# Optimization experiments

Hardware: AMD Instinct MI355X
Metric: run time of the kernel (lower is better)

Reference implementation:

```python
import jax, jax.numpy as jnp
import numpy as np

B, S, HID, NH, HD = 2, 2048, 768, 12, 64
WINDOW = 128           # ModernBERT local attention window
ROPE_THETA = 10000.0   # local_rope_theta (layer_index=0 -> is_local_attention=True)


def _rotate_half(x):
    x1, x2 = jnp.split(x, 2, axis=-1)
    return jnp.concatenate([-x2, x1], axis=-1)


def setup_inputs() -> dict:
    key = jax.random.key(0)
    k1, k2, k3 = jax.random.split(key, 3)
    hidden_embed = jax.random.normal(k1, (B, S, HID), dtype=jnp.float32)
    Wq = jax.random.normal(k2, (HID, HID), dtype=jnp.float32) * (HID ** -0.5)
    Wo = jax.random.normal(k3, (HID, HID), dtype=jnp.float32) * (HID ** -0.5)
    position_index = jnp.arange(S, dtype=jnp.int32).reshape(1, S)
    # sliding-window additive mask: 0 inside window, -inf outside
    i = jnp.arange(S)
    dist = jnp.abs(i[:, None] - i[None, :])
    local_attention_mask = jnp.where(dist <= WINDOW // 2, 0.0, -jnp.inf).astype(jnp.float32)[None, None]
    global_attention_mask = jnp.zeros((1, 1, S, S), dtype=jnp.float32)
    return {
        "hidden_embed": hidden_embed,
        "Wq": Wq,
        "Wo": Wo,
        "local_attention_mask": local_attention_mask,
        "global_attention_mask": global_attention_mask,
        "position_index": position_index,
    }


def reference(hidden_embed, Wq, Wo, local_attention_mask, global_attention_mask, position_index):
    # q projection; NOTE: source has k = q.view(...), v = q.view(...) -> k and v ARE q
    q = hidden_embed @ Wq.T                                  # [B,S,HID]
    q = q.reshape(B, S, NH, HD).transpose(0, 2, 1, 3)        # [B,NH,S,HD]

    # RoPE
    inv_freq = 1.0 / (ROPE_THETA ** (jnp.arange(0, HD, 2, dtype=jnp.float32) / HD))  # [HD/2]
    pos = position_index.reshape(-1).astype(jnp.float32)     # [S]
    freqs = pos[:, None] * inv_freq[None, :]                 # [S,HD/2]
    emb = jnp.concatenate([freqs, freqs], axis=-1)           # [S,HD]
    cos, sin = jnp.cos(emb), jnp.sin(emb)
    q_rot = q * cos + _rotate_half(q) * sin                  # [B,NH,S,HD]
    k_rot = q_rot                                            # k == q before rope -> same after rope
    v = q                                                    # v == q (no rope on v)

    # masked SDPA (local layer -> local sliding-window mask)
    scale = jnp.asarray(HD, jnp.float32) ** -0.5
    scores = jnp.einsum('bhtd,bhsd->bhts', q_rot, k_rot) * scale + local_attention_mask
    attn = jax.nn.softmax(scores, axis=-1)                   # [B,NH,S,S]
    out = jnp.einsum('bhts,bhsd->bhtd', attn, v)             # [B,NH,S,HD]
    out = out.transpose(0, 2, 1, 3).reshape(B, S, HID)
    return out @ Wo.T
```

## Files before the change

### kernel.cpp

```cpp
#include <hip/hip_runtime.h>
#include <hip/hip_bf16.h>
#include <math.h>
#include <stdint.h>

#define B_    2
#define S_    2048
#define HID_  768
#define NH_   12
#define HD_   64
#define NROWS (B_ * S_)
#define N_HID_ELEM (NROWS * HID_)
#define N_W_ELEM   (HID_ * HID_)

#define KW   224
#define KSTR 232

#define TAB_ELEMS (S_ * 32)

typedef __bf16 bf16x8 __attribute__((ext_vector_type(8)));
typedef float  floatx4 __attribute__((ext_vector_type(4)));

__global__ void convert_inputs_kernel(const float* __restrict__ src_hidden,
                                      const float* __restrict__ src_w1,
                                      const float* __restrict__ src_w2,
                                      const int*   __restrict__ pos_idx,
                                      __hip_bfloat16* __restrict__ Hb,
                                      __hip_bfloat16* __restrict__ Wqb,
                                      __hip_bfloat16* __restrict__ Wob,
                                      float2* __restrict__ tab)
{
    int i = blockIdx.x * blockDim.x + threadIdx.x;
    const int NH4 = N_HID_ELEM / 4, NW4 = N_W_ELEM / 4;
    const int total4 = NH4 + 2 * NW4;
    if (i < total4) {
        const float* src;
        __hip_bfloat16* dst;
        int off;
        if (i < NH4)           { src = src_hidden; dst = Hb;  off = i; }
        else if (i < NH4+NW4)  { src = src_w1;     dst = Wqb; off = i - NH4; }
        else                   { src = src_w2;     dst = Wob; off = i - NH4 - NW4; }
        float4 v = reinterpret_cast<const float4*>(src)[off];
        __hip_bfloat16 o[4] = { __float2bfloat16(v.x), __float2bfloat16(v.y),
                                __float2bfloat16(v.z), __float2bfloat16(v.w) };
        *reinterpret_cast<uint64_t*>(dst + 4 * (size_t)off) = *reinterpret_cast<uint64_t*>(o);
    } else {
        int t = i - total4;
        if (t < TAB_ELEMS) {
            int s = t >> 5, f = t & 31;
            float inv = exp2f((float)f * (-0.41524101186092024f));
            float sn, cs;
            sincosf((float)pos_idx[s] * inv, &sn, &cs);
            tab[t] = make_float2(cs, sn);
        }
    }
}

__device__ __forceinline__ void gload_lds16(const __hip_bfloat16* g, __hip_bfloat16* l)
{
    __builtin_amdgcn_global_load_lds(
        (const __attribute__((address_space(1))) void*)g,
        (__attribute__((address_space(3))) void*)l, 16, 0, 0);
}

template<int ROPE>
__global__ __launch_bounds__(512) void gemm64k2(
    const __hip_bfloat16* __restrict__ A,
    const __hip_bfloat16* __restrict__ W,
    __hip_bfloat16* __restrict__ C,
    __hip_bfloat16* __restrict__ C2,
    float* __restrict__ Cf,
    const float2* __restrict__ tab,
    int M, int N, int K)
{
    __shared__ __align__(16) __hip_bfloat16 Ald[2][2][2][64][32];
    __shared__ __align__(16) __hip_bfloat16 Wld[2][2][2][64][32];

    const int tid  = threadIdx.x;
    const int kg   = tid >> 8;
    const int wv4  = (tid >> 6) & 3;
    const int lane = tid & 63;
    const int l16  = lane & 15;
    const int quad = lane >> 4;
    const int m0 = blockIdx.x * 64;
    const int n0 = blockIdx.y * 64;

    const int c    = wv4 * 64 + lane;
    const int sr   = c >> 2;
    const int sc8  = ((c & 3) ^ ((sr >> 1) & 3)) * 8;
    const int kbase = kg * 384;

    const __hip_bfloat16* gA = A + (size_t)(m0 + sr) * K + kbase + sc8;
    const __hip_bfloat16* gW = W + (size_t)(n0 + sr) * K + kbase + sc8;

    floatx4 acc[4] = {};
    const int ra  = wv4 * 16 + l16;
    const int qsw = (quad ^ ((l16 >> 1) & 3)) * 8;

#define STAGE(itx, buf) do {                                          \
        const int ko_ = (itx) * 64;                                   \
        gload_lds16(gA + ko_,      &Ald[kg][buf][0][wv4 * 16][0]);    \
        gload_lds16(gA + ko_ + 32, &Ald[kg][buf][1][wv4 * 16][0]);    \
        gload_lds16(gW + ko_,      &Wld[kg][buf][0][wv4 * 16][0]);    \
        gload_lds16(gW + ko_ + 32, &Wld[kg][buf][1][wv4 * 16][0]);    \
    } while (0)

    STAGE(0, 0);
    STAGE(1, 1);

#pragma unroll
    for (int it = 0; it < 6; ++it) {
        const int cur = it & 1;
        if (it == 5) { asm volatile("s_waitcnt vmcnt(0)" ::: "memory"); }
        else         { asm volatile("s_waitcnt vmcnt(4)" ::: "memory"); }
        __builtin_amdgcn_s_barrier();
        __builtin_amdgcn_sched_barrier(0);
#pragma unroll
        for (int ks = 0; ks < 2; ++ks) {
            bf16x8 a = *reinterpret_cast<const bf16x8*>(&Ald[kg][cur][ks][ra][qsw]);
#pragma unroll
            for (int u = 0; u < 4; ++u) {
                bf16x8 w = *reinterpret_cast<const bf16x8*>(
                    &Wld[kg][cur][ks][u * 16 + l16][qsw]);
                acc[u] = __builtin_amdgcn_mfma_f32_16x16x32_bf16(a, w, acc[u], 0, 0, 0);
            }
        }
        __builtin_amdgcn_sched_barrier(0);
        __builtin_amdgcn_s_barrier();
        if (it + 2 < 6) STAGE(it + 2, cur);
    }
#undef STAGE

    __syncthreads();
    float* Red = reinterpret_cast<float*>(&Ald[0][0][0][0][0]);
    if (kg == 1) {
#pragma unroll
        for (int u = 0; u < 4; ++u)
#pragma unroll
            for (int r = 0; r < 4; ++r)
                Red[(wv4 * 16 + quad * 4 + r) * 68 + u * 16 + l16] = acc[u][r];
    }
    __syncthreads();
    if (kg == 1) return;
#pragma unroll
    for (int u = 0; u < 4; ++u)
#pragma unroll
        for (int r = 0; r < 4; ++r)
            acc[u][r] += Red[(wv4 * 16 + quad * 4 + r) * 68 + u * 16 + l16];

    if (ROPE) {
#pragma unroll
        for (int r = 0; r < 4; ++r) {
            int m = m0 + wv4 * 16 + quad * 4 + r;
            int s = m & (S_ - 1);
#pragma unroll
            for (int u = 0; u < 2; ++u) {
                float2 cssn = tab[s * 32 + u * 16 + l16];
                float cs = cssn.x, sn = cssn.y;
                float q0 = acc[u][r];
                float q1 = acc[u + 2][r];
                size_t base = (size_t)m * HID_ + n0 + u * 16 + l16;
                C [base]      = __float2bfloat16(q0);
                C [base + 32] = __float2bfloat16(q1);
                C2[base]      = __float2bfloat16(q0 * cs - q1 * sn);
                C2[base + 32] = __float2bfloat16(q1 * cs + q0 * sn);
            }
        }
    } else {
#pragma unroll
        for (int u = 0; u < 4; ++u)
#pragma unroll
            for (int r = 0; r < 4; ++r) {
                int row = m0 + wv4 * 16 + quad * 4 + r;
                int col = n0 + u * 16 + l16;
                Cf[(size_t)row * N + col] = acc[u][r];
            }
    }
}

__global__ __launch_bounds__(256) void attn_kernel(
    const __hip_bfloat16* __restrict__ Q,
    const __hip_bfloat16* __restrict__ Qr,
    __hip_bfloat16* __restrict__ O)
{
    __shared__ __align__(16) __hip_bfloat16 Vt[64][KSTR];
    __shared__ __align__(16) __hip_bfloat16 Pl[64][KSTR];

    const int bh = blockIdx.y;
    const int b  = bh / NH_;
    const int h  = bh % NH_;
    const int i0 = blockIdx.x * 64;
    const int tid = threadIdx.x;

    if (tid < KW) {
        int j  = i0 - 64 + tid;
        int jc = min(max(j, 0), S_ - 1);
        const __hip_bfloat16* vrow = Q + ((size_t)(b * S_ + jc)) * HID_ + h * HD_;
#pragma unroll
        for (int d8i = 0; d8i < 8; ++d8i) {
            bf16x8 v = *reinterpret_cast<const bf16x8*>(vrow + d8i * 8);
            const __hip_bfloat16* ve = reinterpret_cast<const __hip_bfloat16*>(&v);
#pragma unroll
            for (int e = 0; e < 8; ++e) Vt[d8i * 8 + e][tid] = ve[e];
        }
    }
    __syncthreads();

    const int wv   = tid >> 6;
    const int lane = tid & 63;
    const int l16  = lane & 15;
    const int quad = lane >> 4;

    floatx4 sc[10] = {};
    const __hip_bfloat16* qrow =
        Qr + ((size_t)(b * S_ + i0 + wv * 16 + l16)) * HID_ + h * HD_ + quad * 8;
#pragma unroll
    for (int ks = 0; ks < 2; ++ks) {
        bf16x8 a = *reinterpret_cast<const bf16x8*>(qrow + ks * 32);
#pragma unroll
        for (int t = 0; t < 10; ++t) {
            int j = i0 - 64 + (wv + t) * 16 + l16;
            int jc = min(max(j, 0), S_ - 1);
            bf16x8 bfr = *reinterpret_cast<const bf16x8*>(
                Qr + ((size_t)(b * S_ + jc)) * HID_ + h * HD_ + ks * 32 + quad * 8);
            sc[t] = __builtin_amdgcn_mfma_f32_16x16x32_bf16(a, bfr, sc[t], 0, 0, 0);
        }
    }

    const float scale = 0.125f;
    float denom[4];
#pragma unroll
    for (int r = 0; r < 4; ++r) {
        const int R = wv * 16 + quad * 4 + r;
        float xv[10];
        float mx = -3.0e38f;
#pragma unroll
        for (int t = 0; t < 10; ++t) {
            int w = (wv + t) * 16 + l16;
            int j = i0 - 64 + w;
            bool valid = (w >= R) && (w <= R + 128) && (j >= 0) && (j < S_);
            float x = valid ? sc[t][r] * scale : -1.0e30f;
            xv[t] = x;
            mx = fmaxf(mx, x);
        }
#pragma unroll
        for (int msk = 1; msk < 16; msk <<= 1) mx = fmaxf(mx, __shfl_xor(mx, msk, 64));
        float sum = 0.f;
#pragma unroll
        for (int t = 0; t < 10; ++t) {
            float p = __expf(xv[t] - mx);
            sum += p;
            Pl[R][(wv + t) * 16 + l16] = __float2bfloat16(p);
        }
#pragma unroll
        for (int msk = 1; msk < 16; msk <<= 1) sum += __shfl_xor(sum, msk, 64);
        denom[r] = sum;
    }
    __syncthreads();

    floatx4 oacc[4] = {};
#pragma unroll
    for (int c = 0; c < 5; ++c) {
        const int base = wv * 16 + c * 32;
        bf16x8 a = *reinterpret_cast<const bf16x8*>(&Pl[wv * 16 + l16][base + quad * 8]);
#pragma unroll
        for (int u = 0; u < 4; ++u) {
            bf16x8 bfr = *reinterpret_cast<const bf16x8*>(&Vt[u * 16 + l16][base + quad * 8]);
            oacc[u] = __builtin_amdgcn_mfma_f32_16x16x32_bf16(a, bfr, oacc[u], 0, 0, 0);
        }
    }

    __syncthreads();
    float* Of = reinterpret_cast<float*>(&Pl[0][0]);
#pragma unroll
    for (int u = 0; u < 4; ++u)
#pragma unroll
        for (int r = 0; r < 4; ++r)
            Of[(wv * 16 + quad * 4 + r) * 68 + u * 16 + l16] = oacc[u][r] / denom[r];
    __syncthreads();
    {
        int row = tid >> 2;
        int seg = (tid & 3) * 16;
        __hip_bfloat16 ob[16];
#pragma unroll
        for (int e = 0; e < 16; ++e)
            ob[e] = __float2bfloat16(Of[row * 68 + seg + e]);
        __hip_bfloat16* dst = O + ((size_t)(b * S_ + i0 + row)) * HID_ + h * HD_ + seg;
        *reinterpret_cast<bf16x8*>(dst)     = *reinterpret_cast<bf16x8*>(ob);
        *reinterpret_cast<bf16x8*>(dst + 8) = *reinterpret_cast<bf16x8*>(ob + 8);
    }
}

extern "C" void kernel_launch(void* const* d_in, const int* in_sizes, int n_in,
                              void* d_out, int out_size, void* d_ws, size_t ws_size,
                              hipStream_t stream)
{
    int ih = -1, iw1 = -1, iw2 = -1, ip = -1;
    for (int i = 0; i < n_in; ++i) {
        int s = in_sizes[i];
        if      (s == N_HID_ELEM && ih < 0) ih = i;
        else if (s == N_W_ELEM)  { if (iw1 < 0) iw1 = i; else if (iw2 < 0) iw2 = i; }
        else if (s == S_ && ip < 0) ip = i;
    }
    if (ih < 0)  ih = 0;
    if (iw1 < 0) iw1 = 1;
    if (iw2 < 0) iw2 = 2;
    if (ip < 0)  ip = 5;

    const float* hidden = (const float*)d_in[ih];
    const float* w1     = (const float*)d_in[iw1];
    const float* w2     = (const float*)d_in[iw2];
    const int*   pos    = (const int*)d_in[ip];

    __hip_bfloat16* Hb  = (__hip_bfloat16*)d_ws;
    __hip_bfloat16* Wqb = Hb  + N_HID_ELEM;
    __hip_bfloat16* Wob = Wqb + N_W_ELEM;
    __hip_bfloat16* Q   = Wob + N_W_ELEM;
    __hip_bfloat16* Qr  = Q   + N_HID_ELEM;
    float2*         Tab = reinterpret_cast<float2*>(Qr + N_HID_ELEM);
    __hip_bfloat16* AO  = Hb;

    int conv4 = (N_HID_ELEM + 2 * N_W_ELEM) / 4;
    int convtot = conv4 + TAB_ELEMS;
    convert_inputs_kernel<<<(convtot + 255) / 256, 256, 0, stream>>>(
        hidden, w1, w2, pos, Hb, Wqb, Wob, Tab);

    dim3 gblk(NROWS / 64, HID_ / 64);

    gemm64k2<1><<<gblk, 512, 0, stream>>>(Hb, Wqb, Q, Qr, nullptr, Tab,
                                          NROWS, HID_, HID_);

    attn_kernel<<<dim3(S_ / 64, B_ * NH_), 256, 0, stream>>>(Q, Qr, AO);

    gemm64k2<0><<<gblk, 512, 0, stream>>>(AO, Wob, nullptr, nullptr, (float*)d_out,
                                          nullptr, NROWS, HID_, HID_);
}
```

Baseline: 139.6 us.

## Fuse fp32-to-bf16 conversion and RoPE table into GEMM kernels

Removes the separate conversion kernel: both GEMMs now load fp32 weights (and fp32 hidden for the Q projection) directly from global memory into registers, convert them to bf16, and write to LDS, with register prefetch replacing async global-to-LDS loads. The RoPE cos/sin table is computed per block in shared memory, and block indices are remapped to group tiles for L2 reuse. This saves one launch and a full bf16 round-trip through memory, at the cost of fetching twice the bytes per GEMM tile, redundant weight conversion across blocks, and extra sincos work per block.

```diff
diff --git a/kernel.cpp b/kernel.cpp
--- a/kernel.cpp
+++ b/kernel.cpp
@@ -15,65 +15,32 @@
 #define KW   224
 #define KSTR 232
 
-#define TAB_ELEMS (S_ * 32)
-
 typedef __bf16 bf16x8 __attribute__((ext_vector_type(8)));
 typedef float  floatx4 __attribute__((ext_vector_type(4)));
 
-__global__ void convert_inputs_kernel(const float* __restrict__ src_hidden,
-                                      const float* __restrict__ src_w1,
-                                      const float* __restrict__ src_w2,
-                                      const int*   __restrict__ pos_idx,
-                                      __hip_bfloat16* __restrict__ Hb,
-                                      __hip_bfloat16* __restrict__ Wqb,
-                                      __hip_bfloat16* __restrict__ Wob,
-                                      float2* __restrict__ tab)
+__device__ __forceinline__ void cvt_write8(const float4& x, const float4& y,
+                                           __hip_bfloat16* d)
 {
-    int i = blockIdx.x * blockDim.x + threadIdx.x;
-    const int NH4 = N_HID_ELEM / 4, NW4 = N_W_ELEM / 4;
-    const int total4 = NH4 + 2 * NW4;
-    if (i < total4) {
-        const float* src;
-        __hip_bfloat16* dst;
-        int off;
-        if (i < NH4)           { src = src_hidden; dst = Hb;  off = i; }
-        else if (i < NH4+NW4)  { src = src_w1;     dst = Wqb; off = i - NH4; }
-        else                   { src = src_w2;     dst = Wob; off = i - NH4 - NW4; }
-        float4 v = reinterpret_cast<const float4*>(src)[off];
-        __hip_bfloat16 o[4] = { __float2bfloat16(v.x), __float2bfloat16(v.y),
-                                __float2bfloat16(v.z), __float2bfloat16(v.w) };
-        *reinterpret_cast<uint64_t*>(dst + 4 * (size_t)off) = *reinterpret_cast<uint64_t*>(o);
-    } else {
-        int t = i - total4;
-        if (t < TAB_ELEMS) {
-            int s = t >> 5, f = t & 31;
-            float inv = exp2f((float)f * (-0.41524101186092024f));
-            float sn, cs;
-            sincosf((float)pos_idx[s] * inv, &sn, &cs);
-            tab[t] = make_float2(cs, sn);
-        }
-    }
+    __hip_bfloat16 t[8] = { __float2bfloat16(x.x), __float2bfloat16(x.y),
+                            __float2bfloat16(x.z), __float2bfloat16(x.w),
+                            __float2bfloat16(y.x), __float2bfloat16(y.y),
+                            __float2bfloat16(y.z), __float2bfloat16(y.w) };
+    *reinterpret_cast<bf16x8*>(d) = *reinterpret_cast<bf16x8*>(t);
 }
 
-__device__ __forceinline__ void gload_lds16(const __hip_bfloat16* g, __hip_bfloat16* l)
-{
-    __builtin_amdgcn_global_load_lds(
-        (const __attribute__((address_space(1))) void*)g,
-        (__attribute__((address_space(3))) void*)l, 16, 0, 0);
-}
-
-template<int ROPE>
-__global__ __launch_bounds__(512) void gemm64k2(
-    const __hip_bfloat16* __restrict__ A,
-    const __hip_bfloat16* __restrict__ W,
+template<int ROPE, int AF32>
+__global__ __launch_bounds__(512, 4) void gemm64f(
+    const void*  __restrict__ Asrc,
+    const float* __restrict__ Wf,
     __hip_bfloat16* __restrict__ C,
     __hip_bfloat16* __restrict__ C2,
     float* __restrict__ Cf,
-    const float2* __restrict__ tab,
-    int M, int N, int K)
+    const int* __restrict__ pos_idx)
 {
+    constexpr int K = HID_;
     __shared__ __align__(16) __hip_bfloat16 Ald[2][2][2][64][32];
     __shared__ __align__(16) __hip_bfloat16 Wld[2][2][2][64][32];
+    __shared__ float2 Rt[64 * 32];
 
     const int tid  = threadIdx.x;
     const int kg   = tid >> 8;
@@ -81,39 +48,81 @@
     const int lane = tid & 63;
     const int l16  = lane & 15;
     const int quad = lane >> 4;
-    const int m0 = blockIdx.x * 64;
-    const int n0 = blockIdx.y * 64;
+
+    const int lin = blockIdx.x + 12 * blockIdx.y;
+    const int o   = (lin & 7) * 96 + (lin >> 3);
+    const int m0  = (o / 12) * 64;
+    const int n0  = (o % 12) * 64;
 
     const int c    = wv4 * 64 + lane;
     const int sr   = c >> 2;
-    const int sc8  = ((c & 3) ^ ((sr >> 1) & 3)) * 8;
-    const int kbase = kg * 384;
-
-    const __hip_bfloat16* gA = A + (size_t)(m0 + sr) * K + kbase + sc8;
-    const __hip_bfloat16* gW = W + (size_t)(n0 + sr) * K + kbase + sc8;
+    const int slot = c & 3;
+    const int sws  = slot ^ ((sr >> 1) & 3);
+    const int kb   = kg * 384;
+
+    const float* pWf = Wf + (size_t)(n0 + sr) * K + kb + sws * 8;
+    const float* pAf = (const float*)Asrc + (size_t)(m0 + sr) * K + kb + sws * 8;
+    const __hip_bfloat16* pAb = (const __hip_bfloat16*)Asrc
+                                + (size_t)(m0 + sr) * K + kb + sws * 8;
+
+    const int dr = wv4 * 16 + (lane >> 2);
+    const int dc = (lane & 3) * 8;
 
     floatx4 acc[4] = {};
     const int ra  = wv4 * 16 + l16;
     const int qsw = (quad ^ ((l16 >> 1) & 3)) * 8;
 
-#define STAGE(itx, buf) do {                                          \
-        const int ko_ = (itx) * 64;                                   \
-        gload_lds16(gA + ko_,      &Ald[kg][buf][0][wv4 * 16][0]);    \
-        gload_lds16(gA + ko_ + 32, &Ald[kg][buf][1][wv4 * 16][0]);    \
-        gload_lds16(gW + ko_,      &Wld[kg][buf][0][wv4 * 16][0]);    \
-        gload_lds16(gW + ko_ + 32, &Wld[kg][buf][1][wv4 * 16][0]);    \
+    float4 rA[2][2];
+    uint4  rAb[2];
+    float4 rW[2][2];
+
+#define LOADR(itx) do {                                                        \
+        const int ko_ = (itx) * 64;                                            \
+        if constexpr (AF32) {                                                  \
+            rA[0][0] = *(const float4*)(pAf + ko_);                            \
+            rA[0][1] = *(const float4*)(pAf + ko_ + 4);                        \
+            rA[1][0] = *(const float4*)(pAf + ko_ + 32);                       \
+            rA[1][1] = *(const float4*)(pAf + ko_ + 36);                       \
+        } else {                                                               \
+            rAb[0] = *(const uint4*)(pAb + ko_);                               \
+            rAb[1] = *(const uint4*)(pAb + ko_ + 32);                          \
+        }                                                                      \
+        rW[0][0] = *(const float4*)(pWf + ko_);                                \
+        rW[0][1] = *(const float4*)(pWf + ko_ + 4);                            \
+        rW[1][0] = *(const float4*)(pWf + ko_ + 32);                           \
+        rW[1][1] = *(const float4*)(pWf + ko_ + 36);                           \
     } while (0)
 
-    STAGE(0, 0);
-    STAGE(1, 1);
+#define WRITES(buf) do {                                                       \
+        if constexpr (AF32) {                                                  \
+            cvt_write8(rA[0][0], rA[0][1], &Ald[kg][buf][0][dr][dc]);          \
+            cvt_write8(rA[1][0], rA[1][1], &Ald[kg][buf][1][dr][dc]);          \
+        } else {                                                               \
+            *reinterpret_cast<uint4*>(&Ald[kg][buf][0][dr][dc]) = rAb[0];      \
+            *reinterpret_cast<uint4*>(&Ald[kg][buf][1][dr][dc]) = rAb[1];      \
+        }                                                                      \
+        cvt_write8(rW[0][0], rW[0][1], &Wld[kg][buf][0][dr][dc]);              \
+        cvt_write8(rW[1][0], rW[1][1], &Wld[kg][buf][1][dr][dc]);              \
+    } while (0)
+
+    LOADR(0);
+    if constexpr (ROPE) {
+        for (int t = tid; t < 64 * 32; t += 512) {
+            int rr = t >> 5, f = t & 31;
+            int s = (m0 + rr) & (S_ - 1);
+            float inv = exp2f((float)f * (-0.41524101186092024f));
+            float sn, cs;
+            sincosf((float)pos_idx[s] * inv, &sn, &cs);
+            Rt[t] = make_float2(cs, sn);
+        }
+    }
+    WRITES(0);
 
 #pragma unroll
     for (int it = 0; it < 6; ++it) {
         const int cur = it & 1;
-        if (it == 5) { asm volatile("s_waitcnt vmcnt(0)" ::: "memory"); }
-        else         { asm volatile("s_waitcnt vmcnt(4)" ::: "memory"); }
-        __builtin_amdgcn_s_barrier();
-        __builtin_amdgcn_sched_barrier(0);
+        __syncthreads();
+        if (it + 1 < 6) LOADR(it + 1);
 #pragma unroll
         for (int ks = 0; ks < 2; ++ks) {
             bf16x8 a = *reinterpret_cast<const bf16x8*>(&Ald[kg][cur][ks][ra][qsw]);
@@ -124,11 +133,10 @@
                 acc[u] = __builtin_amdgcn_mfma_f32_16x16x32_bf16(a, w, acc[u], 0, 0, 0);
             }
         }
-        __builtin_amdgcn_sched_barrier(0);
-        __builtin_amdgcn_s_barrier();
-        if (it + 2 < 6) STAGE(it + 2, cur);
-    }
-#undef STAGE
+        if (it + 1 < 6) WRITES(cur ^ 1);
+    }
+#undef LOADR
+#undef WRITES
 
     __syncthreads();
     float* Red = reinterpret_cast<float*>(&Ald[0][0][0][0][0]);
@@ -147,14 +155,14 @@
         for (int r = 0; r < 4; ++r)
             acc[u][r] += Red[(wv4 * 16 + quad * 4 + r) * 68 + u * 16 + l16];
 
-    if (ROPE) {
+    if constexpr (ROPE) {
 #pragma unroll
         for (int r = 0; r < 4; ++r) {
-            int m = m0 + wv4 * 16 + quad * 4 + r;
-            int s = m & (S_ - 1);
+            int tr = wv4 * 16 + quad * 4 + r;
+            int m  = m0 + tr;
 #pragma unroll
             for (int u = 0; u < 2; ++u) {
-                float2 cssn = tab[s * 32 + u * 16 + l16];
+                float2 cssn = Rt[tr * 32 + u * 16 + l16];
                 float cs = cssn.x, sn = cssn.y;
                 float q0 = acc[u][r];
                 float q1 = acc[u + 2][r];
@@ -172,7 +180,7 @@
             for (int r = 0; r < 4; ++r) {
                 int row = m0 + wv4 * 16 + quad * 4 + r;
                 int col = n0 + u * 16 + l16;
-                Cf[(size_t)row * N + col] = acc[u][r];
+                Cf[(size_t)row * HID_ + col] = acc[u][r];
             }
     }
 }
@@ -311,26 +319,16 @@
     const float* w2     = (const float*)d_in[iw2];
     const int*   pos    = (const int*)d_in[ip];
 
-    __hip_bfloat16* Hb  = (__hip_bfloat16*)d_ws;
-    __hip_bfloat16* Wqb = Hb  + N_HID_ELEM;
-    __hip_bfloat16* Wob = Wqb + N_W_ELEM;
-    __hip_bfloat16* Q   = Wob + N_W_ELEM;
-    __hip_bfloat16* Qr  = Q   + N_HID_ELEM;
-    float2*         Tab = reinterpret_cast<float2*>(Qr + N_HID_ELEM);
-    __hip_bfloat16* AO  = Hb;
-
-    int conv4 = (N_HID_ELEM + 2 * N_W_ELEM) / 4;
-    int convtot = conv4 + TAB_ELEMS;
-    convert_inputs_kernel<<<(convtot + 255) / 256, 256, 0, stream>>>(
-        hidden, w1, w2, pos, Hb, Wqb, Wob, Tab);
-
-    dim3 gblk(NROWS / 64, HID_ / 64);
-
-    gemm64k2<1><<<gblk, 512, 0, stream>>>(Hb, Wqb, Q, Qr, nullptr, Tab,
-                                          NROWS, HID_, HID_);
+    __hip_bfloat16* Q  = (__hip_bfloat16*)d_ws;
+    __hip_bfloat16* Qr = Q  + N_HID_ELEM;
+    __hip_bfloat16* AO = Qr + N_HID_ELEM;
+
+    dim3 gblk(HID_ / 64, NROWS / 64);
+
+    gemm64f<1, 1><<<gblk, 512, 0, stream>>>(hidden, w1, Q, Qr, nullptr, pos);
 
     attn_kernel<<<dim3(S_ / 64, B_ * NH_), 256, 0, stream>>>(Q, Qr, AO);
 
-    gemm64k2<0><<<gblk, 512, 0, stream>>>(AO, Wob, nullptr, nullptr, (float*)d_out,
-                                          nullptr, NROWS, HID_, HID_);
+    gemm64f<0, 0><<<gblk, 512, 0, stream>>>(AO, w2, nullptr, nullptr, (float*)d_out,
+                                            nullptr);
 }
```

Result: slower. 153.3 us (+9.8%).
